# Optimization experiments

Hardware: AMD Instinct MI355X
Metric: run time of the kernel (lower is better)

## Reference

```python
import jax, jax.numpy as jnp
import numpy as np

N = 100_000          # NEURON_COUNT (scaled)
INPUT_SIZE = 1024    # input neurons occupy indices [0, INPUT_SIZE)
OUTPUT_SIZE = 256    # output neurons occupy indices [N-OUTPUT_SIZE, N)
E = 10_000_000       # SYNAPSE_RATIO * N
STEPS = 3


def setup_inputs() -> dict:
    key = jax.random.key(0)
    k1, k2, k3, k4, k5 = jax.random.split(key, 5)
    x = jax.random.normal(k1, (INPUT_SIZE,), dtype=jnp.float32)
    synapse_weights = jax.random.normal(k2, (E,), dtype=jnp.float32)
    neuron_biases = jax.random.normal(k3, (N - INPUT_SIZE,), dtype=jnp.float32)
    synapse_src = jax.random.randint(k4, (E,), 0, N, dtype=jnp.int64) if jax.config.jax_enable_x64 else jax.random.randint(k4, (E,), 0, N, dtype=jnp.int32)
    synapse_dst = jax.random.randint(k5, (E,), 0, N, dtype=jnp.int64) if jax.config.jax_enable_x64 else jax.random.randint(k5, (E,), 0, N, dtype=jnp.int32)
    return {
        "x": x,
        "synapse_weights": synapse_weights,
        "neuron_biases": neuron_biases,
        "synapse_src": synapse_src,
        "synapse_dst": synapse_dst,
    }


def reference(x, synapse_weights, neuron_biases, synapse_src, synapse_dst):
    # Initial state: zeros everywhere, inputs injected at the first INPUT_SIZE slots.
    v = jnp.zeros((N,), dtype=x.dtype).at[:INPUT_SIZE].set(x.reshape(-1))
    # tanh applied to all neurons except outputs (last OUTPUT_SIZE indices)
    tanh_mask = jnp.arange(N) < (N - OUTPUT_SIZE)
    for _ in range(STEPS):
        # vectorized gather-multiply-scatter: next[to] += v[from] * w  (one segment_sum)
        msg = v[synapse_src] * synapse_weights                       # [E]
        nxt = jax.ops.segment_sum(msg, synapse_dst, num_segments=N)  # [N]
        # biases added to all non-input neurons
        nxt = nxt.at[INPUT_SIZE:].add(neuron_biases)
        # tanh everywhere except output neurons
        v = jnp.where(tanh_mask, jnp.tanh(nxt), nxt)
    return v[N - OUTPUT_SIZE:]
```

## Files before the change

### kernel.cpp

```cpp
#include <hip/hip_runtime.h>

#define N_NEURONS   100000
#define INPUT_SIZE  1024
#define OUTPUT_SIZE 256
#define E_SYN       10000000
#define STEPS       3

#define RANGES      8
#define BIN         12500
#define SCAT_BLK    1024
#define CBLK        64
#define RG          8
#define RSL         (CBLK / RG)
#define CAP         1280000
#define VEC4        (E_SYN / 4)

#define CHK         1024
#define NCH         9766
#define PITER       (CHK / 256)
#define PW          4
#define HIST_GRID   ((NCH + PW - 1) / PW)
#define PART_GRID   ((NCH + PW - 1) / PW)
#define SCJ         ((NCH + 1023) / 1024)

__global__ void init_state(const float* __restrict__ x, float* __restrict__ v) {
    int i = blockIdx.x * blockDim.x + threadIdx.x;
    if (i < N_NEURONS) v[i] = (i < INPUT_SIZE) ? x[i] : 0.0f;
}

__global__ __launch_bounds__(256) void hist_kernel(const int* __restrict__ dst,
                                                   int* __restrict__ hist) {
    const int lane  = threadIdx.x & 63;
    const int wv    = threadIdx.x >> 6;
    const int chunk = blockIdx.x * PW + wv;
    if (chunk >= NCH) return;
    const int beg = chunk * CHK;
    const int4* dst4 = (const int4*)dst;
    int h = 0;
    for (int it = 0; it < PITER; ++it) {
        int e   = beg + (it * 64 + lane) * 4;
        bool ok = (e < E_SYN);
        int4 d4 = ok ? dst4[e >> 2] : make_int4(0, 0, 0, 0);
        unsigned long long okm = __ballot(ok);
        int rk[4] = {d4.x / BIN, d4.y / BIN, d4.z / BIN, d4.w / BIN};
#pragma unroll
        for (int k = 0; k < 4; ++k) {
            unsigned long long b0 = __ballot(rk[k] & 1);
            unsigned long long b1 = __ballot(rk[k] & 2);
            unsigned long long b2 = __ballot(rk[k] & 4);
            unsigned long long m = ((lane & 1) ? b0 : ~b0) &
                                   ((lane & 2) ? b1 : ~b1) &
                                   ((lane & 4) ? b2 : ~b2) & okm;
            h += __popcll(m);
        }
    }
    if (lane < RANGES) hist[(size_t)lane * NCH + chunk] = h;
}

__global__ __launch_bounds__(1024) void scan_kernel(const int* __restrict__ hist,
                                                    int* __restrict__ bases,
                                                    int* __restrict__ gcur) {
    const int r = blockIdx.x;
    const int t = threadIdx.x;
    const int lane = t & 63;
    const int wv   = t >> 6;
    int vals[SCJ];
    int s = 0;
#pragma unroll
    for (int j = 0; j < SCJ; ++j) {
        int idx = t * SCJ + j;
        int vv  = (idx < NCH) ? hist[(size_t)r * NCH + idx] : 0;
        vals[j] = vv;
        s += vv;
    }
    int x = s;
#pragma unroll
    for (int d = 1; d < 64; d <<= 1) {
        int y = __shfl_up(x, d, 64);
        if (lane >= d) x += y;
    }
    __shared__ int wsum[16];
    if (lane == 63) wsum[wv] = x;
    __syncthreads();
    if (wv == 0) {
        int y = (lane < 16) ? wsum[lane] : 0;
        int z = y;
#pragma unroll
        for (int d = 1; d < 16; d <<= 1) {
            int u = __shfl_up(z, d, 64);
            if (lane >= d) z += u;
        }
        if (lane < 16) wsum[lane] = z - y;
    }
    __syncthreads();
    int run = (x - s) + wsum[wv];
#pragma unroll
    for (int j = 0; j < SCJ; ++j) {
        int idx = t * SCJ + j;
        if (idx < NCH) bases[(size_t)r * NCH + idx] = r * CAP + run;
        run += vals[j];
    }
    if (t == 1023) gcur[r] = run;
}

__global__ __launch_bounds__(256) void partition_kernel(
        const float* __restrict__ w,
        const int*   __restrict__ src,
        const int*   __restrict__ dst,
        const int*   __restrict__ bases,
        int2* __restrict__ recs) {
    const int lane  = threadIdx.x & 63;
    const int wv    = threadIdx.x >> 6;
    const int chunk = blockIdx.x * PW + wv;
    if (chunk >= NCH) return;
    const unsigned long long ltmask = (1ull << lane) - 1ull;

    int cur = 0;
    if (lane < RANGES) cur = bases[(size_t)lane * NCH + chunk];

    const int beg = chunk * CHK;
    const int4* dst4 = (const int4*)dst;
    const int4* src4 = (const int4*)src;
    const int4* wq4  = (const int4*)w;

    for (int it = 0; it < PITER; ++it) {
        int e   = beg + (it * 64 + lane) * 4;
        bool ok = (e < E_SYN);
        int idx = e >> 2;
        int4 d4 = ok ? dst4[idx] : make_int4(0, 0, 0, 0);
        int4 s4 = ok ? src4[idx] : make_int4(0, 0, 0, 0);
        int4 q4 = ok ? wq4[idx]  : make_int4(0, 0, 0, 0);
        unsigned long long okm = __ballot(ok);
        int dd[4] = {d4.x, d4.y, d4.z, d4.w};
        int ss[4] = {s4.x, s4.y, s4.z, s4.w};
        int qq[4] = {q4.x, q4.y, q4.z, q4.w};
#pragma unroll
        for (int k = 0; k < 4; ++k) {
            int d = dd[k];
            int r = d / BIN;
            unsigned long long b0 = __ballot(r & 1);
            unsigned long long b1 = __ballot(r & 2);
            unsigned long long b2 = __ballot(r & 4);
            unsigned long long mym = ((r & 1) ? b0 : ~b0) &
                                     ((r & 2) ? b1 : ~b1) &
                                     ((r & 4) ? b2 : ~b2) & okm;
            int rank = __popcll(mym & ltmask);
            int gpos = __shfl(cur, r, 64) + rank;
            if (ok) recs[(size_t)gpos] =
                make_int2((ss[k] << 14) | (d - r * BIN), qq[k]);
            unsigned long long mm = ((lane & 1) ? b0 : ~b0) &
                                    ((lane & 2) ? b1 : ~b1) &
                                    ((lane & 4) ? b2 : ~b2) & okm;
            cur += __popcll(mm);
        }
    }
}

__global__ __launch_bounds__(SCAT_BLK) void scatter_sorted(
        const int2* __restrict__ recs,
        const int*  __restrict__ gcur,
        const float* __restrict__ v,
        float* __restrict__ partials) {
    __shared__ float bins[BIN];
    const int r = blockIdx.x / CBLK;
    const int c = blockIdx.x % CBLK;
    for (int j = threadIdx.x; j < BIN; j += SCAT_BLK) bins[j] = 0.0f;
    __syncthreads();

    const int cnt   = gcur[r];
    const int npair = cnt >> 1;
    const int4* base4 = (const int4*)(recs + (size_t)r * CAP);
    const int stride = CBLK * SCAT_BLK;
    int u = c * SCAT_BLK + threadIdx.x;
    for (; u + 3 * stride < npair; u += 4 * stride) {
        int4 a = base4[u];
        int4 b = base4[u + stride];
        int4 e = base4[u + 2 * stride];
        int4 f = base4[u + 3 * stride];
        float va0 = v[a.x >> 14];
        float va1 = v[a.z >> 14];
        float vb0 = v[b.x >> 14];
        float vb1 = v[b.z >> 14];
        float ve0 = v[e.x >> 14];
        float ve1 = v[e.z >> 14];
        float vf0 = v[f.x >> 14];
        float vf1 = v[f.z >> 14];
        atomicAdd(&bins[a.x & 16383], va0 * __int_as_float(a.y));
        atomicAdd(&bins[a.z & 16383], va1 * __int_as_float(a.w));
        atomicAdd(&bins[b.x & 16383], vb0 * __int_as_float(b.y));
        atomicAdd(&bins[b.z & 16383], vb1 * __int_as_float(b.w));
        atomicAdd(&bins[e.x & 16383], ve0 * __int_as_float(e.y));
        atomicAdd(&bins[e.z & 16383], ve1 * __int_as_float(e.w));
        atomicAdd(&bins[f.x & 16383], vf0 * __int_as_float(f.y));
        atomicAdd(&bins[f.z & 16383], vf1 * __int_as_float(f.w));
    }
    for (; u < npair; u += stride) {
        int4 a = base4[u];
        atomicAdd(&bins[a.x & 16383], v[a.x >> 14] * __int_as_float(a.y));
        atomicAdd(&bins[a.z & 16383], v[a.z >> 14] * __int_as_float(a.w));
    }
    if ((cnt & 1) && c == 0 && threadIdx.x == 0) {
        int2 p = recs[(size_t)r * CAP + cnt - 1];
        atomicAdd(&bins[p.x & 16383], v[p.x >> 14] * __int_as_float(p.y));
    }
    __syncthreads();
    float* o = partials + (size_t)(r * CBLK + c) * BIN;
    for (int j = threadIdx.x; j < BIN; j += SCAT_BLK) o[j] = bins[j];
}

__global__ void reduce_fused(const float* __restrict__ partials,
                             const float* __restrict__ bias,
                             float* __restrict__ v,
                             float* __restrict__ out,
                             int write_out) {
    int i4 = 4 * (blockIdx.x * blockDim.x + threadIdx.x);
    if (i4 >= N_NEURONS) return;
    const int r = i4 / BIN;
    const int j = i4 - r * BIN;
    const float* base = partials + (size_t)(r * CBLK) * BIN + j;
    float4 tot = {0.f, 0.f, 0.f, 0.f};
#pragma unroll 2
    for (int g = 0; g < RG; ++g) {
        float4 a = {0.f, 0.f, 0.f, 0.f};
#pragma unroll
        for (int cc = 0; cc < RSL; ++cc) {
            float4 p = *(const float4*)(base + (size_t)(g * RSL + cc) * BIN);
            a.x += p.x; a.y += p.y; a.z += p.z; a.w += p.w;
        }
        tot.x += a.x; tot.y += a.y; tot.z += a.z; tot.w += a.w;
    }
    float av[4] = {tot.x, tot.y, tot.z, tot.w};
#pragma unroll
    for (int k = 0; k < 4; ++k) {
        int i = i4 + k;
        float val = av[k] + ((i >= INPUT_SIZE) ? bias[i - INPUT_SIZE] : 0.0f);
        float nv  = (i < N_NEURONS - OUTPUT_SIZE) ? tanhf(val) : val;
        v[i] = nv;
        if (write_out && i >= N_NEURONS - OUTPUT_SIZE)
            out[i - (N_NEURONS - OUTPUT_SIZE)] = val;
    }
}

__global__ void scatter_binned(const float* __restrict__ w,
                               const int*   __restrict__ src,
                               const int*   __restrict__ dst,
                               const float* __restrict__ v,
                               float*       __restrict__ partials,
                               int C) {
    __shared__ float bins[BIN];
    const int r = blockIdx.x / C;
    const int c = blockIdx.x % C;
    const int lo = r * BIN;
    const int hi = lo + BIN;
    for (int j = threadIdx.x; j < BIN; j += blockDim.x) bins[j] = 0.0f;
    __syncthreads();
    const int4*   src4 = (const int4*)src;
    const int4*   dst4 = (const int4*)dst;
    const float4* w4v  = (const float4*)w;
    const int stride = C * blockDim.x;
    for (int u = c * blockDim.x + threadIdx.x; u < VEC4; u += stride) {
        const int4   s4 = src4[u];
        const int4   d4 = dst4[u];
        const float4 wv = w4v[u];
        int   s[4] = {s4.x, s4.y, s4.z, s4.w};
        int   d[4] = {d4.x, d4.y, d4.z, d4.w};
        float ww[4] = {wv.x, wv.y, wv.z, wv.w};
#pragma unroll
        for (int k = 0; k < 4; ++k)
            if (d[k] >= lo && d[k] < hi)
                atomicAdd(&bins[d[k] - lo], v[s[k]] * ww[k]);
    }
    __syncthreads();
    float* o = partials + ((size_t)(r * C + c)) * BIN;
    for (int j = threadIdx.x; j < BIN; j += blockDim.x) o[j] = bins[j];
}
__global__ void reduce_update_fb(const float* __restrict__ partials,
                                 const float* __restrict__ bias,
                                 float* __restrict__ v,
                                 float* __restrict__ out,
                                 int C, int write_out) {
    int i4 = 4 * (blockIdx.x * blockDim.x + threadIdx.x);
    if (i4 >= N_NEURONS) return;
    const int r = i4 / BIN;
    const int j = i4 - r * BIN;
    const float* base = partials + ((size_t)r * C) * BIN + j;
    float4 acc = {0.f, 0.f, 0.f, 0.f};
    for (int c = 0; c < C; ++c) {
        float4 p = *(const float4*)(base + (size_t)c * BIN);
        acc.x += p.x; acc.y += p.y; acc.z += p.z; acc.w += p.w;
    }
    float av[4] = {acc.x, acc.y, acc.z, acc.w};
#pragma unroll
    for (int k = 0; k < 4; ++k) {
        int i = i4 + k;
        float val = av[k] + ((i >= INPUT_SIZE) ? bias[i - INPUT_SIZE] : 0.0f);
        float nv  = (i < N_NEURONS - OUTPUT_SIZE) ? tanhf(val) : val;
        v[i] = nv;
        if (write_out && i >= N_NEURONS - OUTPUT_SIZE)
            out[i - (N_NEURONS - OUTPUT_SIZE)] = val;
    }
}

extern "C" void kernel_launch(void* const* d_in, const int* in_sizes, int n_in,
                              void* d_out, int out_size, void* d_ws, size_t ws_size,
                              hipStream_t stream) {
    const float* x    = (const float*)d_in[0];
    const float* w    = (const float*)d_in[1];
    const float* bias = (const float*)d_in[2];
    const int*   src  = (const int*)d_in[3];
    const int*   dst  = (const int*)d_in[4];
    float* out = (float*)d_out;

    const int blk = 256;
    const int grid_n   = (N_NEURONS + blk - 1) / blk;
    const int red_grid = (N_NEURONS / 4 + blk - 1) / blk;

    float* v        = (float*)d_ws;
    float* partials = v + N_NEURONS;
    int*   hist     = (int*)(partials + (size_t)RANGES * CBLK * BIN);
    int*   bases    = hist + (size_t)RANGES * NCH;
    int2*  recs     = (int2*)(bases + (size_t)RANGES * NCH);
    int*   gcur     = (int*)(recs + (size_t)RANGES * CAP);
    size_t need = (size_t)((char*)(gcur + RANGES) - (char*)d_ws);

    if (ws_size >= need) {
        init_state<<<grid_n, blk, 0, stream>>>(x, v);
        hist_kernel<<<HIST_GRID, 256, 0, stream>>>(dst, hist);
        scan_kernel<<<RANGES, 1024, 0, stream>>>(hist, bases, gcur);
        partition_kernel<<<PART_GRID, 256, 0, stream>>>(w, src, dst, bases, recs);
        for (int s = 0; s < STEPS; ++s) {
            scatter_sorted<<<RANGES * CBLK, SCAT_BLK, 0, stream>>>(
                recs, gcur, v, partials);
            reduce_fused<<<red_grid, blk, 0, stream>>>(
                partials, bias, v, out, s == STEPS - 1 ? 1 : 0);
        }
    } else {
        long C = (long)(ws_size / 4 / N_NEURONS) - 1;
        if (C > 64) C = 64;
        if (C < 1) C = 1;
        float* part_fb = v + N_NEURONS;
        init_state<<<grid_n, blk, 0, stream>>>(x, v);
        for (int s = 0; s < STEPS; ++s) {
            scatter_binned<<<RANGES * (int)C, SCAT_BLK, 0, stream>>>(
                w, src, dst, v, part_fb, (int)C);
            reduce_update_fb<<<red_grid, blk, 0, stream>>>(
                part_fb, bias, v, out, (int)C, s == STEPS - 1 ? 1 : 0);
        }
    }
}
```

Baseline: 384.5 us.

## Bucket synapses by destination and source range, stage v slices in shared memory

```diff
diff --git a/kernel.cpp b/kernel.cpp
--- a/kernel.cpp
+++ b/kernel.cpp
@@ -6,61 +6,58 @@
 #define E_SYN       10000000
 #define STEPS       3
 
-#define RANGES      8
+#define NR          8
+#define NS          8
+#define NCAT        (NR * NS)
 #define BIN         12500
 #define SCAT_BLK    1024
-#define CBLK        64
+#define CSTRIPE     32
 #define RG          8
-#define RSL         (CBLK / RG)
+#define RSL         (CSTRIPE / RG)
 #define CAP         1280000
 #define VEC4        (E_SYN / 4)
 
-#define CHK         1024
-#define NCH         9766
+#define CHK         2048
+#define NCH         4883
 #define PITER       (CHK / 256)
-#define PW          4
-#define HIST_GRID   ((NCH + PW - 1) / PW)
-#define PART_GRID   ((NCH + PW - 1) / PW)
-#define SCJ         ((NCH + 1023) / 1024)
+#define HP_GRID     ((NCH + 3) / 4)
+#define SCJ         5
 
 __global__ void init_state(const float* __restrict__ x, float* __restrict__ v) {
     int i = blockIdx.x * blockDim.x + threadIdx.x;
     if (i < N_NEURONS) v[i] = (i < INPUT_SIZE) ? x[i] : 0.0f;
 }
 
-__global__ __launch_bounds__(256) void hist_kernel(const int* __restrict__ dst,
+__global__ __launch_bounds__(256) void hist_kernel(const int* __restrict__ src,
+                                                   const int* __restrict__ dst,
                                                    int* __restrict__ hist) {
+    __shared__ int h[4][NCAT];
     const int lane  = threadIdx.x & 63;
     const int wv    = threadIdx.x >> 6;
-    const int chunk = blockIdx.x * PW + wv;
+    const int chunk = blockIdx.x * 4 + wv;
     if (chunk >= NCH) return;
+    h[wv][lane] = 0;
     const int beg = chunk * CHK;
     const int4* dst4 = (const int4*)dst;
-    int h = 0;
+    const int4* src4 = (const int4*)src;
     for (int it = 0; it < PITER; ++it) {
-        int e   = beg + (it * 64 + lane) * 4;
-        bool ok = (e < E_SYN);
-        int4 d4 = ok ? dst4[e >> 2] : make_int4(0, 0, 0, 0);
-        unsigned long long okm = __ballot(ok);
-        int rk[4] = {d4.x / BIN, d4.y / BIN, d4.z / BIN, d4.w / BIN};
-#pragma unroll
-        for (int k = 0; k < 4; ++k) {
-            unsigned long long b0 = __ballot(rk[k] & 1);
-            unsigned long long b1 = __ballot(rk[k] & 2);
-            unsigned long long b2 = __ballot(rk[k] & 4);
-            unsigned long long m = ((lane & 1) ? b0 : ~b0) &
-                                   ((lane & 2) ? b1 : ~b1) &
-                                   ((lane & 4) ? b2 : ~b2) & okm;
-            h += __popcll(m);
-        }
-    }
-    if (lane < RANGES) hist[(size_t)lane * NCH + chunk] = h;
+        int e = beg + (it * 64 + lane) * 4;
+        if (e < E_SYN) {
+            int4 d4 = dst4[e >> 2];
+            int4 s4 = src4[e >> 2];
+            atomicAdd(&h[wv][(d4.x / BIN) * NS + s4.x / BIN], 1);
+            atomicAdd(&h[wv][(d4.y / BIN) * NS + s4.y / BIN], 1);
+            atomicAdd(&h[wv][(d4.z / BIN) * NS + s4.z / BIN], 1);
+            atomicAdd(&h[wv][(d4.w / BIN) * NS + s4.w / BIN], 1);
+        }
+    }
+    hist[(size_t)lane * NCH + chunk] = h[wv][lane];
 }
 
 __global__ __launch_bounds__(1024) void scan_kernel(const int* __restrict__ hist,
                                                     int* __restrict__ bases,
-                                                    int* __restrict__ gcur) {
-    const int r = blockIdx.x;
+                                                    int* __restrict__ gtot) {
+    const int ct = blockIdx.x;
     const int t = threadIdx.x;
     const int lane = t & 63;
     const int wv   = t >> 6;
@@ -69,7 +66,7 @@
 #pragma unroll
     for (int j = 0; j < SCJ; ++j) {
         int idx = t * SCJ + j;
-        int vv  = (idx < NCH) ? hist[(size_t)r * NCH + idx] : 0;
+        int vv  = (idx < NCH) ? hist[(size_t)ct * NCH + idx] : 0;
         vals[j] = vv;
         s += vv;
     }
@@ -97,10 +94,22 @@
 #pragma unroll
     for (int j = 0; j < SCJ; ++j) {
         int idx = t * SCJ + j;
-        if (idx < NCH) bases[(size_t)r * NCH + idx] = r * CAP + run;
+        if (idx < NCH) bases[(size_t)ct * NCH + idx] = run;
         run += vals[j];
     }
-    if (t == 1023) gcur[r] = run;
+    if (t == 1023) gtot[ct] = run;
+}
+
+__global__ void compose_kernel(const int* __restrict__ gtot, int* __restrict__ gstart) {
+    int r = threadIdx.x;
+    if (r < NR) {
+        int s = r * CAP;
+        for (int sb = 0; sb < NS; ++sb) {
+            int c = r * NS + sb;
+            gstart[c] = s;
+            s = (s + gtot[c] + 1) & ~1;
+        }
+    }
 }
 
 __global__ __launch_bounds__(256) void partition_kernel(
@@ -108,104 +117,98 @@
         const int*   __restrict__ src,
         const int*   __restrict__ dst,
         const int*   __restrict__ bases,
+        const int*   __restrict__ gstart,
         int2* __restrict__ recs) {
+    __shared__ int cur[4][NCAT];
     const int lane  = threadIdx.x & 63;
     const int wv    = threadIdx.x >> 6;
-    const int chunk = blockIdx.x * PW + wv;
+    const int chunk = blockIdx.x * 4 + wv;
     if (chunk >= NCH) return;
-    const unsigned long long ltmask = (1ull << lane) - 1ull;
-
-    int cur = 0;
-    if (lane < RANGES) cur = bases[(size_t)lane * NCH + chunk];
-
+    cur[wv][lane] = gstart[lane] + bases[(size_t)lane * NCH + chunk];
     const int beg = chunk * CHK;
     const int4* dst4 = (const int4*)dst;
     const int4* src4 = (const int4*)src;
     const int4* wq4  = (const int4*)w;
-
     for (int it = 0; it < PITER; ++it) {
-        int e   = beg + (it * 64 + lane) * 4;
-        bool ok = (e < E_SYN);
-        int idx = e >> 2;
-        int4 d4 = ok ? dst4[idx] : make_int4(0, 0, 0, 0);
-        int4 s4 = ok ? src4[idx] : make_int4(0, 0, 0, 0);
-        int4 q4 = ok ? wq4[idx]  : make_int4(0, 0, 0, 0);
-        unsigned long long okm = __ballot(ok);
-        int dd[4] = {d4.x, d4.y, d4.z, d4.w};
-        int ss[4] = {s4.x, s4.y, s4.z, s4.w};
-        int qq[4] = {q4.x, q4.y, q4.z, q4.w};
-#pragma unroll
-        for (int k = 0; k < 4; ++k) {
-            int d = dd[k];
-            int r = d / BIN;
-            unsigned long long b0 = __ballot(r & 1);
-            unsigned long long b1 = __ballot(r & 2);
-            unsigned long long b2 = __ballot(r & 4);
-            unsigned long long mym = ((r & 1) ? b0 : ~b0) &
-                                     ((r & 2) ? b1 : ~b1) &
-                                     ((r & 4) ? b2 : ~b2) & okm;
-            int rank = __popcll(mym & ltmask);
-            int gpos = __shfl(cur, r, 64) + rank;
-            if (ok) recs[(size_t)gpos] =
-                make_int2((ss[k] << 14) | (d - r * BIN), qq[k]);
-            unsigned long long mm = ((lane & 1) ? b0 : ~b0) &
-                                    ((lane & 2) ? b1 : ~b1) &
-                                    ((lane & 4) ? b2 : ~b2) & okm;
-            cur += __popcll(mm);
-        }
-    }
-}
-
-__global__ __launch_bounds__(SCAT_BLK) void scatter_sorted(
+        int e = beg + (it * 64 + lane) * 4;
+        if (e < E_SYN) {
+            int4 d4 = dst4[e >> 2];
+            int4 s4 = src4[e >> 2];
+            int4 q4 = wq4[e >> 2];
+            int dd[4] = {d4.x, d4.y, d4.z, d4.w};
+            int ss[4] = {s4.x, s4.y, s4.z, s4.w};
+            int qq[4] = {q4.x, q4.y, q4.z, q4.w};
+#pragma unroll
+            for (int k = 0; k < 4; ++k) {
+                int d = dd[k], s = ss[k];
+                int r = d / BIN;
+                int cat = r * NS + s / BIN;
+                int pos = atomicAdd(&cur[wv][cat], 1);
+                recs[(size_t)pos] = make_int2((s << 14) | (d - r * BIN), qq[k]);
+            }
+        }
+    }
+}
+
+__global__ __launch_bounds__(SCAT_BLK) void scatter_sorted2(
         const int2* __restrict__ recs,
-        const int*  __restrict__ gcur,
+        const int*  __restrict__ gstart,
+        const int*  __restrict__ gtot,
         const float* __restrict__ v,
         float* __restrict__ partials) {
-    __shared__ float bins[BIN];
-    const int r = blockIdx.x / CBLK;
-    const int c = blockIdx.x % CBLK;
-    for (int j = threadIdx.x; j < BIN; j += SCAT_BLK) bins[j] = 0.0f;
-    __syncthreads();
-
-    const int cnt   = gcur[r];
-    const int npair = cnt >> 1;
-    const int4* base4 = (const int4*)(recs + (size_t)r * CAP);
-    const int stride = CBLK * SCAT_BLK;
-    int u = c * SCAT_BLK + threadIdx.x;
-    for (; u + 3 * stride < npair; u += 4 * stride) {
-        int4 a = base4[u];
-        int4 b = base4[u + stride];
-        int4 e = base4[u + 2 * stride];
-        int4 f = base4[u + 3 * stride];
-        float va0 = v[a.x >> 14];
-        float va1 = v[a.z >> 14];
-        float vb0 = v[b.x >> 14];
-        float vb1 = v[b.z >> 14];
-        float ve0 = v[e.x >> 14];
-        float ve1 = v[e.z >> 14];
-        float vf0 = v[f.x >> 14];
-        float vf1 = v[f.z >> 14];
-        atomicAdd(&bins[a.x & 16383], va0 * __int_as_float(a.y));
-        atomicAdd(&bins[a.z & 16383], va1 * __int_as_float(a.w));
-        atomicAdd(&bins[b.x & 16383], vb0 * __int_as_float(b.y));
-        atomicAdd(&bins[b.z & 16383], vb1 * __int_as_float(b.w));
-        atomicAdd(&bins[e.x & 16383], ve0 * __int_as_float(e.y));
-        atomicAdd(&bins[e.z & 16383], ve1 * __int_as_float(e.w));
-        atomicAdd(&bins[f.x & 16383], vf0 * __int_as_float(f.y));
-        atomicAdd(&bins[f.z & 16383], vf1 * __int_as_float(f.w));
-    }
-    for (; u < npair; u += stride) {
-        int4 a = base4[u];
-        atomicAdd(&bins[a.x & 16383], v[a.x >> 14] * __int_as_float(a.y));
-        atomicAdd(&bins[a.z & 16383], v[a.z >> 14] * __int_as_float(a.w));
-    }
-    if ((cnt & 1) && c == 0 && threadIdx.x == 0) {
-        int2 p = recs[(size_t)r * CAP + cnt - 1];
-        atomicAdd(&bins[p.x & 16383], v[p.x >> 14] * __int_as_float(p.y));
-    }
-    __syncthreads();
-    float* o = partials + (size_t)(r * CBLK + c) * BIN;
-    for (int j = threadIdx.x; j < BIN; j += SCAT_BLK) o[j] = bins[j];
+    extern __shared__ float smem[];
+    float* bins = smem;
+    float* vst  = smem + BIN;
+    const int r = blockIdx.x / CSTRIPE;
+    const int c = blockIdx.x % CSTRIPE;
+    const int tid = threadIdx.x;
+    for (int j = tid; j < BIN; j += SCAT_BLK) bins[j] = 0.0f;
+    const int stride = CSTRIPE * SCAT_BLK;
+    for (int sb = 0; sb < NS; ++sb) {
+        __syncthreads();
+        const float4* vs4 = (const float4*)(v + (size_t)sb * BIN);
+        float4* vt4 = (float4*)vst;
+#pragma unroll 4
+        for (int j = tid; j < BIN / 4; j += SCAT_BLK) vt4[j] = vs4[j];
+        __syncthreads();
+        const int start = gstart[r * NS + sb];
+        const int T     = gtot[r * NS + sb];
+        const int P     = T >> 1;
+        const int sbb   = sb * BIN;
+        const int4* base4 = (const int4*)(recs + (size_t)start);
+        int u0 = c * SCAT_BLK + tid;
+        int u1 = u0 + stride;
+        int u2 = u1 + stride;
+        bool k0 = u0 < P, k1 = u1 < P, k2 = u2 < P;
+        int4 a0, a1, a2;
+        if (k0) a0 = base4[u0];
+        if (k1) a1 = base4[u1];
+        if (k2) a2 = base4[u2];
+        if (k0) {
+            atomicAdd(&bins[a0.x & 16383], vst[(a0.x >> 14) - sbb] * __int_as_float(a0.y));
+            atomicAdd(&bins[a0.z & 16383], vst[(a0.z >> 14) - sbb] * __int_as_float(a0.w));
+        }
+        if (k1) {
+            atomicAdd(&bins[a1.x & 16383], vst[(a1.x >> 14) - sbb] * __int_as_float(a1.y));
+            atomicAdd(&bins[a1.z & 16383], vst[(a1.z >> 14) - sbb] * __int_as_float(a1.w));
+        }
+        if (k2) {
+            atomicAdd(&bins[a2.x & 16383], vst[(a2.x >> 14) - sbb] * __int_as_float(a2.y));
+            atomicAdd(&bins[a2.z & 16383], vst[(a2.z >> 14) - sbb] * __int_as_float(a2.w));
+        }
+        for (int u = u2 + stride; u < P; u += stride) {
+            int4 a = base4[u];
+            atomicAdd(&bins[a.x & 16383], vst[(a.x >> 14) - sbb] * __int_as_float(a.y));
+            atomicAdd(&bins[a.z & 16383], vst[(a.z >> 14) - sbb] * __int_as_float(a.w));
+        }
+        if ((T & 1) && c == 0 && tid == 0) {
+            int2 p = recs[(size_t)start + T - 1];
+            atomicAdd(&bins[p.x & 16383], vst[(p.x >> 14) - sbb] * __int_as_float(p.y));
+        }
+    }
+    __syncthreads();
+    float* o = partials + (size_t)(r * CSTRIPE + c) * BIN;
+    for (int j = tid; j < BIN; j += SCAT_BLK) o[j] = bins[j];
 }
 
 __global__ void reduce_fused(const float* __restrict__ partials,
@@ -217,7 +220,7 @@
     if (i4 >= N_NEURONS) return;
     const int r = i4 / BIN;
     const int j = i4 - r * BIN;
-    const float* base = partials + (size_t)(r * CBLK) * BIN + j;
+    const float* base = partials + (size_t)(r * CSTRIPE) * BIN + j;
     float4 tot = {0.f, 0.f, 0.f, 0.f};
 #pragma unroll 2
     for (int g = 0; g < RG; ++g) {
@@ -317,20 +320,29 @@
 
     float* v        = (float*)d_ws;
     float* partials = v + N_NEURONS;
-    int*   hist     = (int*)(partials + (size_t)RANGES * CBLK * BIN);
-    int*   bases    = hist + (size_t)RANGES * NCH;
-    int2*  recs     = (int2*)(bases + (size_t)RANGES * NCH);
-    int*   gcur     = (int*)(recs + (size_t)RANGES * CAP);
-    size_t need = (size_t)((char*)(gcur + RANGES) - (char*)d_ws);
+    int*   hist     = (int*)(partials + (size_t)NR * CSTRIPE * BIN);
+    int*   bases    = hist + (size_t)NCAT * NCH;
+    int2*  recs     = (int2*)(bases + (size_t)NCAT * NCH);
+    int*   gtot     = (int*)(recs + (size_t)NR * CAP);
+    int*   gstart   = gtot + NCAT;
+    size_t need = (size_t)((char*)(gstart + NCAT) - (char*)d_ws);
 
     if (ws_size >= need) {
+        static int attr_set = 0;
+        if (!attr_set) {
+            hipFuncSetAttribute((const void*)scatter_sorted2,
+                                hipFuncAttributeMaxDynamicSharedMemorySize,
+                                2 * BIN * (int)sizeof(float));
+            attr_set = 1;
+        }
         init_state<<<grid_n, blk, 0, stream>>>(x, v);
-        hist_kernel<<<HIST_GRID, 256, 0, stream>>>(dst, hist);
-        scan_kernel<<<RANGES, 1024, 0, stream>>>(hist, bases, gcur);
-        partition_kernel<<<PART_GRID, 256, 0, stream>>>(w, src, dst, bases, recs);
+        hist_kernel<<<HP_GRID, 256, 0, stream>>>(src, dst, hist);
+        scan_kernel<<<NCAT, 1024, 0, stream>>>(hist, bases, gtot);
+        compose_kernel<<<1, 64, 0, stream>>>(gtot, gstart);
+        partition_kernel<<<HP_GRID, 256, 0, stream>>>(w, src, dst, bases, gstart, recs);
         for (int s = 0; s < STEPS; ++s) {
-            scatter_sorted<<<RANGES * CBLK, SCAT_BLK, 0, stream>>>(
-                recs, gcur, v, partials);
+            scatter_sorted2<<<NR * CSTRIPE, SCAT_BLK, 2 * BIN * sizeof(float), stream>>>(
+                recs, gstart, gtot, v, partials);
             reduce_fused<<<red_grid, blk, 0, stream>>>(
                 partials, bias, v, out, s == STEPS - 1 ? 1 : 0);
         }
@@ -341,7 +353,7 @@
         float* part_fb = v + N_NEURONS;
         init_state<<<grid_n, blk, 0, stream>>>(x, v);
         for (int s = 0; s < STEPS; ++s) {
-            scatter_binned<<<RANGES * (int)C, SCAT_BLK, 0, stream>>>(
+            scatter_binned<<<NR * (int)C, SCAT_BLK, 0, stream>>>(
                 w, src, dst, v, part_fb, (int)C);
             reduce_update_fb<<<red_grid, blk, 0, stream>>>(
                 part_fb, bias, v, out, (int)C, s == STEPS - 1 ? 1 : 0);
```

Measured after the change: 485.5 us. 26.3% more time.

## Add second-level sort of synapse records by source block for gather locality

Applied to the files above, without the earlier changes.

```diff
diff --git a/kernel.cpp b/kernel.cpp
--- a/kernel.cpp
+++ b/kernel.cpp
@@ -22,6 +22,11 @@
 #define HIST_GRID   ((NCH + PW - 1) / PW)
 #define PART_GRID   ((NCH + PW - 1) / PW)
 #define SCJ         ((NCH + 1023) / 1024)
+
+#define NSB         32
+#define SBW         (N_NEURONS / NSB)
+#define JB          (CAP / 2048)
+#define B_GRID      ((RANGES * JB + 3) / 4)
 
 __global__ void init_state(const float* __restrict__ x, float* __restrict__ v) {
     int i = blockIdx.x * blockDim.x + threadIdx.x;
@@ -152,6 +157,131 @@
                                     ((lane & 2) ? b1 : ~b1) &
                                     ((lane & 4) ? b2 : ~b2) & okm;
             cur += __popcll(mm);
+        }
+    }
+}
+
+
+__global__ __launch_bounds__(256) void histB_kernel(const int2* __restrict__ recs,
+                                                    const int*  __restrict__ gcur,
+                                                    int* __restrict__ histB) {
+    const int lane = threadIdx.x & 63;
+    const int wv   = threadIdx.x >> 6;
+    const int gid  = blockIdx.x * 4 + wv;
+    if (gid >= RANGES * JB) return;
+    const int r = gid / JB;
+    const int j = gid - r * JB;
+    const int cnt = gcur[r];
+    const int2* rb = recs + (size_t)r * CAP;
+    const int base = j * 2048;
+    int h = 0;
+    const int c = lane & 31;
+    for (int it = 0; it < 32; ++it) {
+        int idx = base + it * 64 + lane;
+        bool ok = idx < cnt;
+        int rx  = ok ? rb[idx].x : 0;
+        int sb  = (rx >> 14) / SBW;
+        unsigned long long okm = __ballot(ok);
+        unsigned long long b0 = __ballot(sb & 1);
+        unsigned long long b1 = __ballot(sb & 2);
+        unsigned long long b2 = __ballot(sb & 4);
+        unsigned long long b3 = __ballot(sb & 8);
+        unsigned long long b4 = __ballot(sb & 16);
+        unsigned long long m = ((c & 1) ? b0 : ~b0) & ((c & 2) ? b1 : ~b1) &
+                               ((c & 4) ? b2 : ~b2) & ((c & 8) ? b3 : ~b3) &
+                               ((c & 16) ? b4 : ~b4) & okm;
+        h += __popcll(m);
+    }
+    if (lane < NSB) histB[(size_t)(r * NSB + lane) * JB + j] = h;
+}
+
+__global__ __launch_bounds__(64) void scanB_kernel(const int* __restrict__ histB,
+                                                   int* __restrict__ basesB,
+                                                   int* __restrict__ totB) {
+    const int cat  = blockIdx.x;
+    const int lane = threadIdx.x;
+    int vals[10];
+    int s = 0;
+#pragma unroll
+    for (int j = 0; j < 10; ++j) {
+        int idx = lane * 10 + j;
+        int vv  = (idx < JB) ? histB[(size_t)cat * JB + idx] : 0;
+        vals[j] = vv;
+        s += vv;
+    }
+    int x = s;
+#pragma unroll
+    for (int d = 1; d < 64; d <<= 1) {
+        int y = __shfl_up(x, d, 64);
+        if (lane >= d) x += y;
+    }
+    int run = x - s;
+#pragma unroll
+    for (int j = 0; j < 10; ++j) {
+        int idx = lane * 10 + j;
+        if (idx < JB) basesB[(size_t)cat * JB + idx] = run;
+        run += vals[j];
+    }
+    if (lane == 63) totB[cat] = x;
+}
+
+__global__ void composeB_kernel(const int* __restrict__ totB,
+                                int* __restrict__ gstartB) {
+    int r = threadIdx.x;
+    if (r < RANGES) {
+        int s = r * CAP;
+        for (int sb = 0; sb < NSB; ++sb) {
+            gstartB[r * NSB + sb] = s;
+            s += totB[r * NSB + sb];
+        }
+    }
+}
+
+__global__ __launch_bounds__(256) void partB_kernel(const int2* __restrict__ recs,
+                                                    const int*  __restrict__ gcur,
+                                                    const int*  __restrict__ basesB,
+                                                    const int*  __restrict__ gstartB,
+                                                    int2* __restrict__ recs2) {
+    const int lane = threadIdx.x & 63;
+    const int wv   = threadIdx.x >> 6;
+    const int gid  = blockIdx.x * 4 + wv;
+    if (gid >= RANGES * JB) return;
+    const int r = gid / JB;
+    const int j = gid - r * JB;
+    const int cnt = gcur[r];
+    if (j * 2048 >= cnt) return;
+    const unsigned long long ltmask = (1ull << lane) - 1ull;
+    int cur = 0;
+    if (lane < NSB)
+        cur = gstartB[r * NSB + lane] + basesB[(size_t)(r * NSB + lane) * JB + j];
+    const int4* rb4 = (const int4*)(recs + (size_t)r * CAP + (size_t)j * 2048);
+    for (int it = 0; it < 16; ++it) {
+        int pi  = it * 64 + lane;
+        int idx = j * 2048 + pi * 2;
+        int4 p  = rb4[pi];
+#pragma unroll
+        for (int k = 0; k < 2; ++k) {
+            bool ok = (idx + k) < cnt;
+            int rx = k ? p.z : p.x;
+            int ry = k ? p.w : p.y;
+            int sb = (rx >> 14) / SBW;
+            unsigned long long okm = __ballot(ok);
+            unsigned long long b0 = __ballot(sb & 1);
+            unsigned long long b1 = __ballot(sb & 2);
+            unsigned long long b2 = __ballot(sb & 4);
+            unsigned long long b3 = __ballot(sb & 8);
+            unsigned long long b4 = __ballot(sb & 16);
+            unsigned long long mym = ((sb & 1) ? b0 : ~b0) & ((sb & 2) ? b1 : ~b1) &
+                                     ((sb & 4) ? b2 : ~b2) & ((sb & 8) ? b3 : ~b3) &
+                                     ((sb & 16) ? b4 : ~b4) & okm;
+            int rank = __popcll(mym & ltmask);
+            int gpos = __shfl(cur, sb, 64) + rank;
+            if (ok) recs2[(size_t)gpos] = make_int2(rx, ry);
+            const int c = lane & 31;
+            unsigned long long mm = ((c & 1) ? b0 : ~b0) & ((c & 2) ? b1 : ~b1) &
+                                    ((c & 4) ? b2 : ~b2) & ((c & 8) ? b3 : ~b3) &
+                                    ((c & 16) ? b4 : ~b4) & okm;
+            if (lane < NSB) cur += __popcll(mm);
         }
     }
 }
@@ -317,20 +447,35 @@
 
     float* v        = (float*)d_ws;
     float* partials = v + N_NEURONS;
-    int*   hist     = (int*)(partials + (size_t)RANGES * CBLK * BIN);
-    int*   bases    = hist + (size_t)RANGES * NCH;
-    int2*  recs     = (int2*)(bases + (size_t)RANGES * NCH);
-    int*   gcur     = (int*)(recs + (size_t)RANGES * CAP);
-    size_t need = (size_t)((char*)(gcur + RANGES) - (char*)d_ws);
-
-    if (ws_size >= need) {
+    int*   histA    = (int*)(partials + (size_t)RANGES * CBLK * BIN);
+    int*   basesA   = histA + (size_t)RANGES * NCH;
+    int*   histB    = basesA + (size_t)RANGES * NCH;
+    int*   basesB   = histB + (size_t)RANGES * NSB * JB;
+    int*   totB     = basesB + (size_t)RANGES * NSB * JB;
+    int*   gstartB  = totB + RANGES * NSB;
+    int*   gcur     = gstartB + RANGES * NSB;
+    int2*  recs     = (int2*)(gcur + RANGES);
+    int2*  recs2    = recs + (size_t)RANGES * CAP;
+    size_t need_sorted = (size_t)((char*)recs2 - (char*)d_ws);
+    size_t need_full   = (size_t)((char*)(recs2 + (size_t)RANGES * CAP) - (char*)d_ws);
+
+    if (ws_size >= need_sorted) {
+        const bool subsort = (ws_size >= need_full);
         init_state<<<grid_n, blk, 0, stream>>>(x, v);
-        hist_kernel<<<HIST_GRID, 256, 0, stream>>>(dst, hist);
-        scan_kernel<<<RANGES, 1024, 0, stream>>>(hist, bases, gcur);
-        partition_kernel<<<PART_GRID, 256, 0, stream>>>(w, src, dst, bases, recs);
+        hist_kernel<<<HIST_GRID, 256, 0, stream>>>(dst, histA);
+        scan_kernel<<<RANGES, 1024, 0, stream>>>(histA, basesA, gcur);
+        partition_kernel<<<PART_GRID, 256, 0, stream>>>(w, src, dst, basesA, recs);
+        const int2* srecs = recs;
+        if (subsort) {
+            histB_kernel<<<B_GRID, 256, 0, stream>>>(recs, gcur, histB);
+            scanB_kernel<<<RANGES * NSB, 64, 0, stream>>>(histB, basesB, totB);
+            composeB_kernel<<<1, 64, 0, stream>>>(totB, gstartB);
+            partB_kernel<<<B_GRID, 256, 0, stream>>>(recs, gcur, basesB, gstartB, recs2);
+            srecs = recs2;
+        }
         for (int s = 0; s < STEPS; ++s) {
             scatter_sorted<<<RANGES * CBLK, SCAT_BLK, 0, stream>>>(
-                recs, gcur, v, partials);
+                srecs, gcur, v, partials);
             reduce_fused<<<red_grid, blk, 0, stream>>>(
                 partials, bias, v, out, s == STEPS - 1 ? 1 : 0);
         }
```

Result: slower. 489.7 us (+27.4%).

## Split destinations into 16 ranges with smaller LDS bins and fuse init

Applied to the files above, without the earlier changes.

```diff
diff --git a/kernel.cpp b/kernel.cpp
--- a/kernel.cpp
+++ b/kernel.cpp
@@ -6,13 +6,15 @@
 #define E_SYN       10000000
 #define STEPS       3
 
-#define RANGES      8
-#define BIN         12500
-#define SCAT_BLK    1024
+#define RANGES      16
+#define BIN         6250
+#define SHIFT       13
+#define DMASK       8191
+#define SCAT_BLK    512
 #define CBLK        64
 #define RG          8
 #define RSL         (CBLK / RG)
-#define CAP         1280000
+#define CAP         665600
 #define VEC4        (E_SYN / 4)
 
 #define CHK         1024
@@ -20,16 +22,18 @@
 #define PITER       (CHK / 256)
 #define PW          4
 #define HIST_GRID   ((NCH + PW - 1) / PW)
-#define PART_GRID   ((NCH + PW - 1) / PW)
 #define SCJ         ((NCH + 1023) / 1024)
 
-__global__ void init_state(const float* __restrict__ x, float* __restrict__ v) {
-    int i = blockIdx.x * blockDim.x + threadIdx.x;
-    if (i < N_NEURONS) v[i] = (i < INPUT_SIZE) ? x[i] : 0.0f;
-}
-
-__global__ __launch_bounds__(256) void hist_kernel(const int* __restrict__ dst,
+#define CMB(x, b0, b1, b2, b3) \
+    ((((x) & 1) ? (b0) : ~(b0)) & (((x) & 2) ? (b1) : ~(b1)) & \
+     (((x) & 4) ? (b2) : ~(b2)) & (((x) & 8) ? (b3) : ~(b3)))
+
+__global__ __launch_bounds__(256) void hist_kernel(const float* __restrict__ x,
+                                                   float* __restrict__ v,
+                                                   const int* __restrict__ dst,
                                                    int* __restrict__ hist) {
+    const int gidx = blockIdx.x * 256 + threadIdx.x;
+    if (gidx < N_NEURONS) v[gidx] = (gidx < INPUT_SIZE) ? x[gidx] : 0.0f;
     const int lane  = threadIdx.x & 63;
     const int wv    = threadIdx.x >> 6;
     const int chunk = blockIdx.x * PW + wv;
@@ -48,10 +52,8 @@
             unsigned long long b0 = __ballot(rk[k] & 1);
             unsigned long long b1 = __ballot(rk[k] & 2);
             unsigned long long b2 = __ballot(rk[k] & 4);
-            unsigned long long m = ((lane & 1) ? b0 : ~b0) &
-                                   ((lane & 2) ? b1 : ~b1) &
-                                   ((lane & 4) ? b2 : ~b2) & okm;
-            h += __popcll(m);
+            unsigned long long b3 = __ballot(rk[k] & 8);
+            h += __popcll(CMB(lane, b0, b1, b2, b3) & okm);
         }
     }
     if (lane < RANGES) hist[(size_t)lane * NCH + chunk] = h;
@@ -141,16 +143,13 @@
             unsigned long long b0 = __ballot(r & 1);
             unsigned long long b1 = __ballot(r & 2);
             unsigned long long b2 = __ballot(r & 4);
-            unsigned long long mym = ((r & 1) ? b0 : ~b0) &
-                                     ((r & 2) ? b1 : ~b1) &
-                                     ((r & 4) ? b2 : ~b2) & okm;
+            unsigned long long b3 = __ballot(r & 8);
+            unsigned long long mym = CMB(r, b0, b1, b2, b3) & okm;
             int rank = __popcll(mym & ltmask);
             int gpos = __shfl(cur, r, 64) + rank;
             if (ok) recs[(size_t)gpos] =
-                make_int2((ss[k] << 14) | (d - r * BIN), qq[k]);
-            unsigned long long mm = ((lane & 1) ? b0 : ~b0) &
-                                    ((lane & 2) ? b1 : ~b1) &
-                                    ((lane & 4) ? b2 : ~b2) & okm;
+                make_int2((ss[k] << SHIFT) | (d - r * BIN), qq[k]);
+            unsigned long long mm = CMB(lane, b0, b1, b2, b3) & okm;
             cur += __popcll(mm);
         }
     }
@@ -164,48 +163,45 @@
     __shared__ float bins[BIN];
     const int r = blockIdx.x / CBLK;
     const int c = blockIdx.x % CBLK;
-    for (int j = threadIdx.x; j < BIN; j += SCAT_BLK) bins[j] = 0.0f;
+    const int tid = threadIdx.x;
+    for (int j = tid; j < BIN; j += SCAT_BLK) bins[j] = 0.0f;
     __syncthreads();
 
     const int cnt   = gcur[r];
     const int npair = cnt >> 1;
     const int4* base4 = (const int4*)(recs + (size_t)r * CAP);
     const int stride = CBLK * SCAT_BLK;
-    int u = c * SCAT_BLK + threadIdx.x;
+    int u = c * SCAT_BLK + tid;
     for (; u + 3 * stride < npair; u += 4 * stride) {
-        int4 a = base4[u];
-        int4 b = base4[u + stride];
-        int4 e = base4[u + 2 * stride];
-        int4 f = base4[u + 3 * stride];
-        float va0 = v[a.x >> 14];
-        float va1 = v[a.z >> 14];
-        float vb0 = v[b.x >> 14];
-        float vb1 = v[b.z >> 14];
-        float ve0 = v[e.x >> 14];
-        float ve1 = v[e.z >> 14];
-        float vf0 = v[f.x >> 14];
-        float vf1 = v[f.z >> 14];
-        atomicAdd(&bins[a.x & 16383], va0 * __int_as_float(a.y));
-        atomicAdd(&bins[a.z & 16383], va1 * __int_as_float(a.w));
-        atomicAdd(&bins[b.x & 16383], vb0 * __int_as_float(b.y));
-        atomicAdd(&bins[b.z & 16383], vb1 * __int_as_float(b.w));
-        atomicAdd(&bins[e.x & 16383], ve0 * __int_as_float(e.y));
-        atomicAdd(&bins[e.z & 16383], ve1 * __int_as_float(e.w));
-        atomicAdd(&bins[f.x & 16383], vf0 * __int_as_float(f.y));
-        atomicAdd(&bins[f.z & 16383], vf1 * __int_as_float(f.w));
+        int4 A[4];
+#pragma unroll
+        for (int i = 0; i < 4; ++i) A[i] = base4[u + i * stride];
+        float g[8];
+#pragma unroll
+        for (int i = 0; i < 4; ++i) {
+            g[2 * i]     = v[A[i].x >> SHIFT];
+            g[2 * i + 1] = v[A[i].z >> SHIFT];
+        }
+#pragma unroll
+        for (int i = 0; i < 4; ++i) {
+            atomicAdd(&bins[A[i].x & DMASK], g[2 * i]     * __int_as_float(A[i].y));
+            atomicAdd(&bins[A[i].z & DMASK], g[2 * i + 1] * __int_as_float(A[i].w));
+        }
     }
     for (; u < npair; u += stride) {
         int4 a = base4[u];
-        atomicAdd(&bins[a.x & 16383], v[a.x >> 14] * __int_as_float(a.y));
-        atomicAdd(&bins[a.z & 16383], v[a.z >> 14] * __int_as_float(a.w));
-    }
-    if ((cnt & 1) && c == 0 && threadIdx.x == 0) {
+        float v0 = v[a.x >> SHIFT];
+        float v1 = v[a.z >> SHIFT];
+        atomicAdd(&bins[a.x & DMASK], v0 * __int_as_float(a.y));
+        atomicAdd(&bins[a.z & DMASK], v1 * __int_as_float(a.w));
+    }
+    if ((cnt & 1) && c == 0 && tid == 0) {
         int2 p = recs[(size_t)r * CAP + cnt - 1];
-        atomicAdd(&bins[p.x & 16383], v[p.x >> 14] * __int_as_float(p.y));
-    }
-    __syncthreads();
-    float* o = partials + (size_t)(r * CBLK + c) * BIN;
-    for (int j = threadIdx.x; j < BIN; j += SCAT_BLK) o[j] = bins[j];
+        atomicAdd(&bins[p.x & DMASK], v[p.x >> SHIFT] * __int_as_float(p.y));
+    }
+    __syncthreads();
+    float* o = partials + (size_t)c * N_NEURONS + r * BIN;
+    for (int j = tid; j < BIN; j += SCAT_BLK) o[j] = bins[j];
 }
 
 __global__ void reduce_fused(const float* __restrict__ partials,
@@ -215,16 +211,14 @@
                              int write_out) {
     int i4 = 4 * (blockIdx.x * blockDim.x + threadIdx.x);
     if (i4 >= N_NEURONS) return;
-    const int r = i4 / BIN;
-    const int j = i4 - r * BIN;
-    const float* base = partials + (size_t)(r * CBLK) * BIN + j;
+    const float* base = partials + i4;
     float4 tot = {0.f, 0.f, 0.f, 0.f};
 #pragma unroll 2
     for (int g = 0; g < RG; ++g) {
         float4 a = {0.f, 0.f, 0.f, 0.f};
 #pragma unroll
         for (int cc = 0; cc < RSL; ++cc) {
-            float4 p = *(const float4*)(base + (size_t)(g * RSL + cc) * BIN);
+            float4 p = *(const float4*)(base + (size_t)(g * RSL + cc) * N_NEURONS);
             a.x += p.x; a.y += p.y; a.z += p.z; a.w += p.w;
         }
         tot.x += a.x; tot.y += a.y; tot.z += a.z; tot.w += a.w;
@@ -241,6 +235,10 @@
     }
 }
 
+__global__ void init_state_fb(const float* __restrict__ x, float* __restrict__ v) {
+    int i = blockIdx.x * blockDim.x + threadIdx.x;
+    if (i < N_NEURONS) v[i] = (i < INPUT_SIZE) ? x[i] : 0.0f;
+}
 __global__ void scatter_binned(const float* __restrict__ w,
                                const int*   __restrict__ src,
                                const int*   __restrict__ dst,
@@ -271,7 +269,7 @@
                 atomicAdd(&bins[d[k] - lo], v[s[k]] * ww[k]);
     }
     __syncthreads();
-    float* o = partials + ((size_t)(r * C + c)) * BIN;
+    float* o = partials + (size_t)c * N_NEURONS + r * BIN;
     for (int j = threadIdx.x; j < BIN; j += blockDim.x) o[j] = bins[j];
 }
 __global__ void reduce_update_fb(const float* __restrict__ partials,
@@ -281,12 +279,10 @@
                                  int C, int write_out) {
     int i4 = 4 * (blockIdx.x * blockDim.x + threadIdx.x);
     if (i4 >= N_NEURONS) return;
-    const int r = i4 / BIN;
-    const int j = i4 - r * BIN;
-    const float* base = partials + ((size_t)r * C) * BIN + j;
+    const float* base = partials + i4;
     float4 acc = {0.f, 0.f, 0.f, 0.f};
     for (int c = 0; c < C; ++c) {
-        float4 p = *(const float4*)(base + (size_t)c * BIN);
+        float4 p = *(const float4*)(base + (size_t)c * N_NEURONS);
         acc.x += p.x; acc.y += p.y; acc.z += p.z; acc.w += p.w;
     }
     float av[4] = {acc.x, acc.y, acc.z, acc.w};
@@ -317,17 +313,16 @@
 
     float* v        = (float*)d_ws;
     float* partials = v + N_NEURONS;
-    int*   hist     = (int*)(partials + (size_t)RANGES * CBLK * BIN);
+    int*   hist     = (int*)(partials + (size_t)CBLK * N_NEURONS);
     int*   bases    = hist + (size_t)RANGES * NCH;
-    int2*  recs     = (int2*)(bases + (size_t)RANGES * NCH);
-    int*   gcur     = (int*)(recs + (size_t)RANGES * CAP);
-    size_t need = (size_t)((char*)(gcur + RANGES) - (char*)d_ws);
+    int*   gcur     = bases + (size_t)RANGES * NCH;
+    int2*  recs     = (int2*)(gcur + RANGES);
+    size_t need = (size_t)((char*)(recs + (size_t)RANGES * CAP) - (char*)d_ws);
 
     if (ws_size >= need) {
-        init_state<<<grid_n, blk, 0, stream>>>(x, v);
-        hist_kernel<<<HIST_GRID, 256, 0, stream>>>(dst, hist);
+        hist_kernel<<<HIST_GRID, 256, 0, stream>>>(x, v, dst, hist);
         scan_kernel<<<RANGES, 1024, 0, stream>>>(hist, bases, gcur);
-        partition_kernel<<<PART_GRID, 256, 0, stream>>>(w, src, dst, bases, recs);
+        partition_kernel<<<HIST_GRID, 256, 0, stream>>>(w, src, dst, bases, recs);
         for (int s = 0; s < STEPS; ++s) {
             scatter_sorted<<<RANGES * CBLK, SCAT_BLK, 0, stream>>>(
                 recs, gcur, v, partials);
@@ -339,7 +334,7 @@
         if (C > 64) C = 64;
         if (C < 1) C = 1;
         float* part_fb = v + N_NEURONS;
-        init_state<<<grid_n, blk, 0, stream>>>(x, v);
+        init_state_fb<<<grid_n, blk, 0, stream>>>(x, v);
         for (int s = 0; s < STEPS; ++s) {
             scatter_binned<<<RANGES * (int)C, SCAT_BLK, 0, stream>>>(
                 w, src, dst, v, part_fb, (int)C);
```

After: 397.7 us. +3.4%, slower.
